# Optimization experiments

Hardware: AMD Instinct MI355X
Metric: run time of the kernel (lower is better)

The kernel has to match this reference:

```python
import jax, jax.numpy as jnp
import numpy as np

B, S, D, H = 4, 1024, 1024, 16
HD = D // H          # head space dim = 64
FF = 4 * D           # ffn hidden = 4096
EPS = 1e-6

# ---- Lorentz manifold helpers (curvature k=1: -t^2 + |s|^2 = -1) ----

def to_manifold(space):
    t = jnp.sqrt(jnp.sum(space * space, -1, keepdims=True) + 1.0)
    return jnp.concatenate([t, space], -1)

def l_inner(x, y):
    return -x[..., 0] * y[..., 0] + jnp.sum(x[..., 1:] * y[..., 1:], -1)

def project(z):
    # renormalize onto hyperboloid: z / sqrt(|<z,z>_L|)   (Lorentz midpoint / LResNet)
    d = jnp.sqrt(jnp.clip(-l_inner(z, z), EPS))
    return z / d[..., None]

def hyp_layernorm(x, g, b):
    s = x[..., 1:]
    mu = jnp.mean(s, -1, keepdims=True)
    var = jnp.var(s, -1, keepdims=True)
    s = (s - mu) * jax.lax.rsqrt(var + 1e-5) * g + b
    return to_manifold(s)

def apply_rope(xs, cos, sin):
    # xs [B,S,H,HD]; cos/sin [S,HD//2]; freqs broadcast as [1,S,1,HD//2]
    x2 = xs.reshape(*xs.shape[:-1], HD // 2, 2)
    c = cos[None, :, None, :]
    s = sin[None, :, None, :]
    xr = x2[..., 0] * c - x2[..., 1] * s
    xi = x2[..., 0] * s + x2[..., 1] * c
    return jnp.stack([xr, xi], -1).reshape(xs.shape)


def setup_inputs() -> dict:
    key = jax.random.key(0)
    ks = jax.random.split(key, 8)
    def w(k, shape, fan_in):
        return jax.random.normal(k, shape, jnp.float32) / np.sqrt(fan_in).astype(np.float32)
    x = to_manifold(0.5 * jax.random.normal(ks[0], (B, S, D), jnp.float32))
    pos = jnp.arange(S, dtype=jnp.float32)[:, None]
    inv = 1.0 / (10000.0 ** (jnp.arange(0, HD, 2, dtype=jnp.float32) / HD))
    ang = pos * inv[None, :]
    return {
        'x': x,
        'rope_cos': jnp.cos(ang), 'rope_sin': jnp.sin(ang),
        'norm1_g': jnp.ones((D,), jnp.float32), 'norm1_b': jnp.zeros((D,), jnp.float32),
        'Wq': w(ks[1], (H, D + 1, HD), D + 1), 'bq': jnp.zeros((H, HD), jnp.float32),
        'Wk': w(ks[2], (H, D + 1, HD), D + 1), 'bk': jnp.zeros((H, HD), jnp.float32),
        'Wv': w(ks[3], (H, D + 1, HD), D + 1), 'bv': jnp.zeros((H, HD), jnp.float32),
        'attn_scale': jnp.asarray(np.sqrt(HD), jnp.float32),
        'attn_bias': jnp.zeros((), jnp.float32),
        'Wo': w(ks[4], (H * (HD + 1), D), H * (HD + 1)), 'bo': jnp.zeros((D,), jnp.float32),
        'w_res1': jnp.asarray(1.0, jnp.float32),
        'norm2_g': jnp.ones((D,), jnp.float32), 'norm2_b': jnp.zeros((D,), jnp.float32),
        'W1': w(ks[5], (D + 1, FF), D + 1), 'b1': jnp.zeros((FF,), jnp.float32),
        'W2': w(ks[6], (FF + 1, D), FF + 1), 'b2': jnp.zeros((D,), jnp.float32),
        'w_res2': jnp.asarray(1.0, jnp.float32),
    }


def reference(x, rope_cos, rope_sin, norm1_g, norm1_b, Wq, bq, Wk, bk, Wv, bv,
              attn_scale, attn_bias, Wo, bo, w_res1, norm2_g, norm2_b,
              W1, b1, W2, b2, w_res2):
    # ---- pre-norm ----
    xn = hyp_layernorm(x, norm1_g, norm1_b)
    # ---- per-head Lorentz linear (space part), inline RoPE on q/k ----
    qs = jnp.einsum('bsd,hde->bshe', xn, Wq) + bq          # [B,S,H,HD]
    ksp = jnp.einsum('bsd,hde->bshe', xn, Wk) + bk
    vsp = jnp.einsum('bsd,hde->bshe', xn, Wv) + bv
    qs = apply_rope(qs, rope_cos, rope_sin)
    ksp = apply_rope(ksp, rope_cos, rope_sin)
    # hyperbolic normalization of q/k: unit space norm, time recomputed
    qs = qs * jax.lax.rsqrt(jnp.sum(qs * qs, -1, keepdims=True) + EPS)
    ksp = ksp * jax.lax.rsqrt(jnp.sum(ksp * ksp, -1, keepdims=True) + EPS)
    q = to_manifold(qs)                                    # [B,S,H,HD+1]
    k = to_manifold(ksp)
    v = to_manifold(vsp)
    # ---- curvature-aware scores: 2 + 2 <q,k>_L (neg sq Lorentz distance) ----
    sgn = jnp.concatenate([-jnp.ones((1,), q.dtype), jnp.ones((HD,), q.dtype)])
    cin = jnp.einsum('bshe,bthe->bhst', q * sgn, k)        # Minkowski inner [B,H,S,S]
    att = (2.0 + 2.0 * cin) / attn_scale + attn_bias
    P = jax.nn.softmax(att, axis=-1)
    # ---- Lorentz midpoint aggregation of values ----
    m = jnp.einsum('bhst,bthe->bshe', P, v)
    m = project(m)                                         # back onto hyperboloid
    # ---- heads concat + output Lorentz linear ----
    cat = m.reshape(B, S, H * (HD + 1))
    attn_out = to_manifold(cat @ Wo + bo)
    # ---- LResNet residual 1 ----
    x = project(x + w_res1 * attn_out)
    # ---- Lorentz FFN ----
    h = hyp_layernorm(x, norm2_g, norm2_b)
    h = to_manifold(jax.nn.gelu(h @ W1 + b1))
    mlp = to_manifold(h @ W2 + b2)
    # ---- LResNet residual 2 ----
    x = project(x + w_res2 * mlp)
    return x
```

## Files before the change

kernel.cpp:

```cpp
#include <hip/hip_runtime.h>
#include <hip/hip_bf16.h>

typedef __hip_bfloat16 bf16;
typedef __attribute__((ext_vector_type(8))) short short8;
typedef __attribute__((ext_vector_type(4))) float f32x4;

#define B_  4
#define S_  1024
#define H_  16
#define R_  4096

#define MBL 1048576L
#define OFF_WQKVT (0L)
#define OFF_X2    (0L)
#define OFF_WOT   (6L*MBL + MBL/2)
#define OFF_W1T   (9L*MBL)
#define OFF_W2T   (17L*MBL + MBL/2)
#define OFF_BIAS  (26L*MBL)
#define OFF_XNB   (27L*MBL)
#define OFF_MCAT  (27L*MBL)
#define OFF_MLP   (27L*MBL)
#define OFF_QPS   (36L*MBL)
#define OFF_ARAW  (36L*MBL)
#define OFF_QT    (44L*MBL)
#define OFF_KPS   (45L*MBL)
#define OFF_HBUF  (45L*MBL)
#define OFF_KT    (53L*MBL)
#define OFF_VT    (54L*MBL)
#define OFF_HHC   (54L*MBL)
#define OFF_HHBIG (54L*MBL)
#define BQKV 0
#define BOF  16384
#define B1F  32768
#define B2F  65536
#define W2R0 81920
#define RCF  98304
#define RSNF 262144
#define SCLF 409600
#define TACC 425984
#define FLAG 458752

__device__ __forceinline__ bf16  f2bf(float v) { return __float2bfloat16(v); }
__device__ __forceinline__ float bf2f(bf16 v)  { return __bfloat162float(v); }
__device__ __forceinline__ unsigned short bf2s(float v) {
  return __builtin_bit_cast(unsigned short, __float2bfloat16(v));
}
__device__ __forceinline__ float ldu(const void* p, long i, int isbf) {
  return isbf ? bf2f(((const bf16*)p)[i]) : ((const float*)p)[i];
}
__device__ __forceinline__ void stu(void* p, long i, float v, int isbf) {
  if (isbf) ((bf16*)p)[i] = f2bf(v);
  else      ((float*)p)[i] = v;
}
__device__ __forceinline__ float gelu_f(float v) {
  const float u = 0.7978845608028654f * (v + 0.044715f * v * v * v);
  const float e = __expf(fminf(2.f * u, 80.f));
  return 0.5f * v * (1.f + (e - 1.f) / (e + 1.f));
}
__device__ __forceinline__ float bfu_lo(unsigned u) {
  return __builtin_bit_cast(float, u << 16);
}
__device__ __forceinline__ float bfu_hi(unsigned u) {
  return __builtin_bit_cast(float, u & 0xFFFF0000u);
}

__device__ __forceinline__ void gload16(const bf16* g, short* l) {
  __builtin_amdgcn_global_load_lds(
      (const __attribute__((address_space(1))) unsigned int*)g,
      (__attribute__((address_space(3))) unsigned int*)l, 16, 0, 0);
}

__global__ void detect_kernel(const unsigned* __restrict__ g, int* __restrict__ flag) {
  if (threadIdx.x == 0) flag[0] = (g[0] == 0x3F803F80u) ? 1 : 0;
}

__global__ __launch_bounds__(256) void zero16_kernel(uint4* __restrict__ p, int n16) {
  int i = blockIdx.x * 256 + threadIdx.x;
  if (i < n16) p[i] = uint4{0, 0, 0, 0};
}

__global__ __launch_bounds__(256) void prep_misc(
    const void* bq, const void* bk, const void* bv, const void* bo, const void* b1,
    const void* b2, const void* W2, const void* rc, const void* rsn,
    const void* scl, const void* ab, const void* wr1, const void* wr2,
    char* bias_base, const int* __restrict__ flag) {
  const int isbf = flag[0];
  int i = blockIdx.x * 256 + threadIdx.x;
  float* bqkvf = (float*)(bias_base + BQKV);
  if (i < 1024)        { bqkvf[i] = ldu(bq, i, isbf); return; }
  if (i < 2048)        { bqkvf[i] = ldu(bk, i - 1024, isbf); return; }
  if (i < 3072)        { bqkvf[i] = ldu(bv, i - 2048, isbf); return; }
  if (i < 4096)        { ((float*)(bias_base + BOF))[i - 3072] = ldu(bo, i - 3072, isbf); return; }
  if (i < 8192)        { ((float*)(bias_base + B1F))[i - 4096] = ldu(b1, i - 4096, isbf); return; }
  if (i < 9216)        { ((float*)(bias_base + B2F))[i - 8192] = ldu(b2, i - 8192, isbf); return; }
  if (i < 10240)       { ((float*)(bias_base + W2R0))[i - 9216] = ldu(W2, i - 9216, isbf); return; }
  if (i < 10240+32768) { ((float*)(bias_base + RCF))[i - 10240] = ldu(rc, i - 10240, isbf); return; }
  if (i < 10240+65536) { ((float*)(bias_base + RSNF))[i - 43008] = ldu(rsn, i - 43008, isbf); return; }
  if (i == 75776)      { ((float*)(bias_base + SCLF))[0] = ldu(scl, 0, isbf); return; }
  if (i == 75777)      { ((float*)(bias_base + SCLF))[1] = ldu(ab, 0, isbf); return; }
  if (i == 75778)      { ((float*)(bias_base + SCLF))[2] = ldu(wr1, 0, isbf); return; }
  if (i == 75779)      { ((float*)(bias_base + SCLF))[3] = ldu(wr2, 0, isbf); return; }
}

__global__ __launch_bounds__(256) void transp_gen(const void* __restrict__ src, long src_off,
                                                  int src_rows, int src_ld,
                                                  bf16* __restrict__ dst, int dst_ld,
                                                  const int* __restrict__ flag) {
  const int isbf = flag[0];
  __shared__ float tl[64][65];
  int t = threadIdx.x, tx = t & 63, tg = t >> 6;
  int k0 = blockIdx.x * 64, n0 = blockIdx.y * 64;
  for (int i = tg; i < 64; i += 4) {
    int k = k0 + i;
    tl[i][tx] = (k < src_rows) ? ldu(src, src_off + (long)k * src_ld + n0 + tx, isbf) : 0.f;
  }
  __syncthreads();
  for (int i = tg; i < 64; i += 4) {
    int k = k0 + tx;
    if (k < dst_ld) dst[(long)(n0 + i) * dst_ld + k] = f2bf(tl[tx][i]);
  }
}

__global__ __launch_bounds__(256) void transp_qkv(const void* __restrict__ Wq,
                                                  const void* __restrict__ Wk,
                                                  const void* __restrict__ Wv,
                                                  bf16* __restrict__ dst,
                                                  const int* __restrict__ flag) {
  const int isbf = flag[0];
  __shared__ float tl[64][65];
  int t = threadIdx.x, tx = t & 63, tg = t >> 6;
  int k0 = blockIdx.x * 64;
  int z = blockIdx.y, mode = z >> 4, h = z & 15;
  const void* src = (mode == 0) ? Wq : (mode == 1) ? Wk : Wv;
  const long soff = (long)h * 1025 * 64;
  int base_n = mode * 1024 + h * 64;
  for (int i = tg; i < 64; i += 4) {
    int k = k0 + i;
    tl[i][tx] = (k < 1025) ? ldu(src, soff + (long)k * 64 + tx, isbf) : 0.f;
  }
  __syncthreads();
  for (int i = tg; i < 64; i += 4) {
    int k = k0 + tx;
    if (k < 1056) dst[(long)(base_n + i) * 1056 + k] = f2bf(tl[tx][i]);
  }
}

__global__ __launch_bounds__(256) void transp_wo(const void* __restrict__ src,
                                                 bf16* __restrict__ dst,
                                                 const int* __restrict__ flag) {
  const int isbf = flag[0];
  __shared__ float tl[64][65];
  int t = threadIdx.x, tx = t & 63, tg = t >> 6;
  int k0 = blockIdx.x * 64, n0 = blockIdx.y * 64;
  for (int i = tg; i < 64; i += 4) {
    int kp = k0 + i;
    int h = kp / 66, e = kp - h * 66;
    float v = 0.f;
    if (kp < 1056 && e < 65) v = ldu(src, (long)(h * 65 + e) * 1024 + n0 + tx, isbf);
    tl[i][tx] = v;
  }
  __syncthreads();
  for (int i = tg; i < 64; i += 4) {
    int kp = k0 + tx;
    if (kp < 1056) dst[(long)(n0 + i) * 1056 + kp] = f2bf(tl[tx][i]);
  }
}

__device__ __forceinline__ float bred_f(float v, float* sh) {
#pragma unroll
  for (int o = 32; o; o >>= 1) v += __shfl_xor(v, o);
  __syncthreads();
  if ((threadIdx.x & 63) == 0) sh[threadIdx.x >> 6] = v;
  __syncthreads();
  return sh[0] + sh[1] + sh[2] + sh[3];
}
__device__ __forceinline__ double bred_d(double v, double* sh) {
#pragma unroll
  for (int o = 32; o; o >>= 1) v += __shfl_xor(v, o);
  __syncthreads();
  if ((threadIdx.x & 63) == 0) sh[threadIdx.x >> 6] = v;
  __syncthreads();
  return sh[0] + sh[1] + sh[2] + sh[3];
}

__global__ __launch_bounds__(256) void ln_kernel(const void* __restrict__ x, int xtag,
                                                 const void* __restrict__ g,
                                                 const void* __restrict__ b,
                                                 bf16* __restrict__ out,
                                                 const int* __restrict__ flag) {
  const int isbf = flag[0];
  const int xb = (xtag == 2) ? isbf : xtag;
  __shared__ float red[4];
  const long base = (long)blockIdx.x * 1025;
  const long obase = (long)blockIdx.x * 1056;
  const int tid = threadIdx.x;
  float v[4];
#pragma unroll
  for (int i = 0; i < 4; i++) v[i] = ldu(x, base + 1 + tid * 4 + i, xb);
  float s = 0.f, s2 = 0.f;
#pragma unroll
  for (int i = 0; i < 4; i++) { s += v[i]; s2 += v[i] * v[i]; }
  s  = bred_f(s,  red);
  s2 = bred_f(s2, red);
  const float mu  = s * (1.f / 1024.f);
  const float var = s2 * (1.f / 1024.f) - mu * mu;
  const float rs  = rsqrtf(var + 1e-5f);
  float n[4], ns = 0.f;
#pragma unroll
  for (int i = 0; i < 4; i++) {
    const int e = tid * 4 + i;
    n[i] = (v[i] - mu) * rs * ldu(g, e, isbf) + ldu(b, e, isbf);
    ns += n[i] * n[i];
  }
  ns = bred_f(ns, red);
  if (tid == 0) out[obase] = f2bf(sqrtf(ns + 1.f));
#pragma unroll
  for (int i = 0; i < 4; i++) out[obase + 1 + tid * 4 + i] = f2bf(n[i]);
  if (tid < 31) out[obase + 1025 + tid] = f2bf(0.f);
}

template <int EPI, bool SS>
__global__ __launch_bounds__(256) void mfma_gemm(const bf16* __restrict__ A, int lda,
                                                 const bf16* __restrict__ Bw, int ldb, int K,
                                                 const float* __restrict__ bias,
                                                 void* __restrict__ Cv, int ldc, int accf,
                                                 float* __restrict__ tacc) {
  __shared__ __align__(16) short As[128 * 32];
  __shared__ __align__(16) short Bs[64 * 32];
  const int tid = threadIdx.x, lane = tid & 63, wv = tid >> 6;
  const int quad = lane >> 4, q15 = lane & 15;
  const int wave_m = wv & 1, wave_n = wv >> 1;
  const int n0 = blockIdx.x * 64, m0 = blockIdx.y * 128;
  const int sa0 = wv * 128 + lane, sa1 = sa0 + 64;
  const int ra0 = sa0 >> 2, ca0 = (sa0 & 3) ^ (ra0 & 3);
  const int ra1 = sa1 >> 2, ca1 = (sa1 & 3) ^ (ra1 & 3);
  const int rb = tid >> 2, cb = (tid & 3) ^ (rb & 3);
  const int kswz = (quad ^ (q15 & 3)) * 8;
  const bf16* pa0 = A + (long)(m0 + ra0) * lda + ca0 * 8;
  const bf16* pa1 = A + (long)(m0 + ra1) * lda + ca1 * 8;
  const bf16* pb  = Bw + (long)(n0 + rb) * ldb + cb * 8;
  f32x4 acc[4][2] = {};
  for (int k0 = 0; k0 < K; k0 += 32) {
    gload16(pa0, As + sa0 * 8);
    gload16(pa1, As + sa1 * 8);
    gload16(pb, Bs + tid * 8);
    pa0 += 32; pa1 += 32; pb += 32;
    __syncthreads();
    short8 af[4], bfr[2];
#pragma unroll
    for (int i = 0; i < 4; i++)
      af[i] = *(const short8*)(As + (wave_m * 64 + i * 16 + q15) * 32 + kswz);
#pragma unroll
    for (int i = 0; i < 2; i++)
      bfr[i] = *(const short8*)(Bs + (wave_n * 32 + i * 16 + q15) * 32 + kswz);
#pragma unroll
    for (int mi = 0; mi < 4; mi++)
#pragma unroll
      for (int ni = 0; ni < 2; ni++)
        acc[mi][ni] = __builtin_amdgcn_mfma_f32_16x16x32_bf16(af[mi], bfr[ni], acc[mi][ni], 0, 0, 0);
    __syncthreads();
  }
#pragma unroll
  for (int mi = 0; mi < 4; mi++) {
#pragma unroll
    for (int r = 0; r < 4; r++) {
      const int m = m0 + wave_m * 64 + mi * 16 + quad * 4 + r;
      float s2 = 0.f;
#pragma unroll
      for (int ni = 0; ni < 2; ni++) {
        const int n = n0 + wave_n * 32 + ni * 16 + q15;
        float v = acc[mi][ni][r] + (bias ? bias[n] : 0.f);
        const long idx = (long)m * ldc + n;
        if (EPI == 0) {
          float* Cf = (float*)Cv;
          if (accf) v += Cf[idx];
          Cf[idx] = v;
        } else if (EPI == 1) {
          ((bf16*)Cv)[idx] = f2bf(v);
        } else {
          v = gelu_f(v);
          ((bf16*)Cv)[idx] = f2bf(v);
        }
        if (SS) s2 += v * v;
      }
      if (SS) {
        s2 += __shfl_xor(s2, 1);
        s2 += __shfl_xor(s2, 2);
        s2 += __shfl_xor(s2, 4);
        s2 += __shfl_xor(s2, 8);
        if (q15 == 0) atomicAdd(tacc + m, s2);
      }
    }
  }
}

template <int EPI>
__global__ __launch_bounds__(256) void mfma_gemm128(const bf16* __restrict__ A, int lda,
                                                    const bf16* __restrict__ Bw, int ldb, int K,
                                                    const float* __restrict__ bias,
                                                    void* __restrict__ Cv, int ldc, int accf) {
  __shared__ __align__(16) short As[128 * 32];
  __shared__ __align__(16) short Bs[128 * 32];
  const int tid = threadIdx.x, lane = tid & 63, wv = tid >> 6;
  const int quad = lane >> 4, q15 = lane & 15;
  const int wave_m = wv & 1, wave_n = wv >> 1;
  const int n0 = blockIdx.x * 128, m0 = blockIdx.y * 128;
  const int s0 = wv * 128 + lane, s1 = s0 + 64;
  const int r0 = s0 >> 2, c0 = (s0 & 3) ^ (r0 & 3);
  const int r1 = s1 >> 2, c1 = (s1 & 3) ^ (r1 & 3);
  const int kswz = (quad ^ (q15 & 3)) * 8;
  const bf16* pa0 = A + (long)(m0 + r0) * lda + c0 * 8;
  const bf16* pa1 = A + (long)(m0 + r1) * lda + c1 * 8;
  const bf16* pb0 = Bw + (long)(n0 + r0) * ldb + c0 * 8;
  const bf16* pb1 = Bw + (long)(n0 + r1) * ldb + c1 * 8;
  f32x4 acc[4][4] = {};
  for (int k0 = 0; k0 < K; k0 += 32) {
    gload16(pa0, As + s0 * 8);
    gload16(pa1, As + s1 * 8);
    gload16(pb0, Bs + s0 * 8);
    gload16(pb1, Bs + s1 * 8);
    pa0 += 32; pa1 += 32; pb0 += 32; pb1 += 32;
    __syncthreads();
    short8 af[4], bfr[4];
#pragma unroll
    for (int i = 0; i < 4; i++) {
      af[i]  = *(const short8*)(As + (wave_m * 64 + i * 16 + q15) * 32 + kswz);
      bfr[i] = *(const short8*)(Bs + (wave_n * 64 + i * 16 + q15) * 32 + kswz);
    }
#pragma unroll
    for (int mi = 0; mi < 4; mi++)
#pragma unroll
      for (int ni = 0; ni < 4; ni++)
        acc[mi][ni] = __builtin_amdgcn_mfma_f32_16x16x32_bf16(af[mi], bfr[ni], acc[mi][ni], 0, 0, 0);
    __syncthreads();
  }
#pragma unroll
  for (int mi = 0; mi < 4; mi++) {
#pragma unroll
    for (int r = 0; r < 4; r++) {
      const int m = m0 + wave_m * 64 + mi * 16 + quad * 4 + r;
#pragma unroll
      for (int ni = 0; ni < 4; ni++) {
        const int n = n0 + wave_n * 64 + ni * 16 + q15;
        float v = acc[mi][ni][r] + (bias ? bias[n] : 0.f);
        const long idx = (long)m * ldc + n;
        if (EPI == 0) {
          float* Cf = (float*)Cv;
          if (accf) v += Cf[idx];
          Cf[idx] = v;
        } else if (EPI == 1) {
          ((bf16*)Cv)[idx] = f2bf(v);
        } else {
          ((bf16*)Cv)[idx] = f2bf(gelu_f(v));
        }
      }
    }
  }
}

__global__ __launch_bounds__(256) void gemm_qkv(const bf16* __restrict__ A,
                                                const bf16* __restrict__ Wt,
                                                const char* __restrict__ bias_base,
                                                bf16* __restrict__ qPs, float* __restrict__ qtc,
                                                bf16* __restrict__ kPs, float* __restrict__ ktc,
                                                bf16* __restrict__ vT) {
  __shared__ __align__(16) short As[128 * 32];
  __shared__ __align__(16) short Bs[128 * 32];
  const int tid = threadIdx.x, lane = tid & 63, wv = tid >> 6;
  const int quad = lane >> 4, q15 = lane & 15;
  const int wave_m = wv & 1, wave_n = wv >> 1;
  const int n0 = blockIdx.x * 128, m0 = blockIdx.y * 128;
  const int s0 = wv * 128 + lane, s1 = s0 + 64;
  const int r0 = s0 >> 2, c0 = (s0 & 3) ^ (r0 & 3);
  const int r1 = s1 >> 2, c1 = (s1 & 3) ^ (r1 & 3);
  const int kswz = (quad ^ (q15 & 3)) * 8;
  const float* bqkvf = (const float*)(bias_base + BQKV);
  const float* rcf   = (const float*)(bias_base + RCF);
  const float* rsnf  = (const float*)(bias_base + RSNF);
  const bf16* pa0 = A + (long)(m0 + r0) * 1056 + c0 * 8;
  const bf16* pa1 = A + (long)(m0 + r1) * 1056 + c1 * 8;
  const bf16* pb0 = Wt + (long)(n0 + r0) * 1056 + c0 * 8;
  const bf16* pb1 = Wt + (long)(n0 + r1) * 1056 + c1 * 8;
  f32x4 acc[4][4] = {};
  for (int k0 = 0; k0 < 1056; k0 += 32) {
    gload16(pa0, As + s0 * 8);
    gload16(pa1, As + s1 * 8);
    gload16(pb0, Bs + s0 * 8);
    gload16(pb1, Bs + s1 * 8);
    pa0 += 32; pa1 += 32; pb0 += 32; pb1 += 32;
    __syncthreads();
    short8 af[4], bfr[4];
#pragma unroll
    for (int i = 0; i < 4; i++) {
      af[i]  = *(const short8*)(As + (wave_m * 64 + i * 16 + q15) * 32 + kswz);
      bfr[i] = *(const short8*)(Bs + (wave_n * 64 + i * 16 + q15) * 32 + kswz);
    }
#pragma unroll
    for (int mi = 0; mi < 4; mi++)
#pragma unroll
      for (int ni = 0; ni < 4; ni++)
        acc[mi][ni] = __builtin_amdgcn_mfma_f32_16x16x32_bf16(af[mi], bfr[ni], acc[mi][ni], 0, 0, 0);
    __syncthreads();
  }
  const int hg = (n0 >> 6) + wave_n;
  const int mode = hg >> 4, h = hg & 15;
  const int nb = hg * 64;
#pragma unroll
  for (int mi = 0; mi < 4; mi++) {
#pragma unroll
    for (int r = 0; r < 4; r++) {
      const int m = m0 + wave_m * 64 + mi * 16 + quad * 4 + r;
      const int bb = m >> 10, s = m & 1023;
      const int bh = bb * H_ + h;
      float v[4];
#pragma unroll
      for (int ns = 0; ns < 4; ns++) v[ns] = acc[mi][ns][r] + bqkvf[nb + ns * 16 + q15];
      if (mode < 2) {
#pragma unroll
        for (int ns = 0; ns < 4; ns++) {
          const int eg = ns * 16 + q15;
          const int j = eg >> 1;
          const float c = rcf[s * 32 + j], sn = rsnf[s * 32 + j];
          const float p = __shfl_xor(v[ns], 1);
          v[ns] = ((eg & 1) == 0) ? (v[ns] * c - p * sn) : (p * sn + v[ns] * c);
        }
      }
      float ss = v[0] * v[0] + v[1] * v[1] + v[2] * v[2] + v[3] * v[3];
#pragma unroll
      for (int o = 8; o; o >>= 1) ss += __shfl_xor(ss, o);
      if (mode == 0) {
        const float sc = rsqrtf(ss + 1e-6f);
        const long rb = (long)(bh * 1024 + s) * 64;
#pragma unroll
        for (int ns = 0; ns < 4; ns++) qPs[rb + ns * 16 + q15] = f2bf(v[ns] * sc);
        if (q15 == 0) qtc[bh * 1024 + s] = sqrtf(ss / (ss + 1e-6f) + 1.f);
      } else if (mode == 1) {
        const float sc = rsqrtf(ss + 1e-6f);
        const long rb = (long)(bh * 1024 + s) * 64;
#pragma unroll
        for (int ns = 0; ns < 4; ns++) kPs[rb + ns * 16 + q15] = f2bf(v[ns] * sc);
        if (q15 == 0) ktc[bh * 1024 + s] = sqrtf(ss / (ss + 1e-6f) + 1.f);
      } else {
        const long vb = (long)bh * 81920;
#pragma unroll
        for (int ns = 0; ns < 4; ns++) vT[vb + (long)(1 + ns * 16 + q15) * 1024 + s] = f2bf(v[ns]);
        if (q15 == 0) vT[vb + s] = f2bf(sqrtf(ss + 1.f));
      }
    }
  }
}

__global__ __launch_bounds__(256) void attn_kernel(const bf16* __restrict__ qPs,
                                                   const float* __restrict__ qtc,
                                                   const bf16* __restrict__ kPs,
                                                   const float* __restrict__ ktc,
                                                   const bf16* __restrict__ vT,
                                                   const float* __restrict__ scalf,
                                                   bf16* __restrict__ mcat) {
  __shared__ __align__(16) short kbuf[64 * 72];
  __shared__ __align__(16) short vbuf[80 * 72];
  __shared__ __align__(16) short pbuf[64 * 72];
  __shared__ float tkl[64];
  const int tid = threadIdx.x, lane = tid & 63, wv = tid >> 6;
  const int quad = lane >> 4, q15 = lane & 15;
  const int id = blockIdx.x;
  const int cxd = id & 7, jj_ = id >> 3;
  const int bh = cxd * 8 + (jj_ & 7), qt_ = jj_ >> 3;
  const float inv_scale = 1.f / scalf[0];
  const long qrow = (long)(bh * 1024 + qt_ * 64 + wv * 16 + q15) * 64;
  const short8 aq0 = *(const short8*)(qPs + qrow + quad * 8);
  const short8 aq1 = *(const short8*)(qPs + qrow + 32 + quad * 8);
  float tqr[4];
#pragma unroll
  for (int r = 0; r < 4; r++) tqr[r] = qtc[bh * 1024 + qt_ * 64 + wv * 16 + quad * 4 + r];
  f32x4 out[5];
#pragma unroll
  for (int mt = 0; mt < 5; mt++) out[mt] = f32x4{0, 0, 0, 0};
  float lip[4] = {0.f, 0.f, 0.f, 0.f};
  const int srcl = (q15 >> 2) << 4;
  for (int kt = 0; kt < 16; kt++) {
    __syncthreads();
#pragma unroll
    for (int c = 0; c < 2; c++) {
      const int id2 = c * 256 + tid, row = id2 >> 3, off = id2 & 7;
      *(uint4*)(kbuf + row * 72 + off * 8) =
          *(const uint4*)(kPs + (long)(bh * 1024 + kt * 64 + row) * 64 + off * 8);
    }
#pragma unroll
    for (int c = 0; c < 3; c++) {
      const int id2 = c * 256 + tid;
      if (id2 < 640) {
        const int row = id2 >> 3, off = id2 & 7;
        *(uint4*)(vbuf + row * 72 + off * 8) =
            *(const uint4*)(vT + (long)bh * 81920 + (long)row * 1024 + kt * 64 + off * 8);
      }
    }
    if (tid < 64) tkl[tid] = ktc[bh * 1024 + kt * 64 + tid];
    __syncthreads();
    f32x4 sacc[4] = {f32x4{0,0,0,0}, f32x4{0,0,0,0}, f32x4{0,0,0,0}, f32x4{0,0,0,0}};
#pragma unroll
    for (int ns = 0; ns < 4; ns++) {
      short8 b0 = *(const short8*)(kbuf + (ns * 16 + q15) * 72 + quad * 8);
      short8 b1 = *(const short8*)(kbuf + (ns * 16 + q15) * 72 + 32 + quad * 8);
      sacc[ns] = __builtin_amdgcn_mfma_f32_16x16x32_bf16(aq0, b0, sacc[ns], 0, 0, 0);
      sacc[ns] = __builtin_amdgcn_mfma_f32_16x16x32_bf16(aq1, b1, sacc[ns], 0, 0, 0);
    }
#pragma unroll
    for (int ns = 0; ns < 4; ns++) {
      const float tk = tkl[ns * 16 + q15];
#pragma unroll
      for (int r = 0; r < 4; r++) {
        const float pv = __expf((2.f + 2.f * (sacc[ns][r] - tqr[r] * tk)) * inv_scale);
        lip[r] += pv;
        pbuf[(wv * 16 + quad * 4 + r) * 72 + ns * 16 + q15] = (short)bf2s(pv);
      }
    }
#pragma unroll
    for (int mt = 0; mt < 5; mt++)
#pragma unroll
      for (int kc = 0; kc < 2; kc++) {
        short8 av = *(const short8*)(vbuf + (mt * 16 + q15) * 72 + kc * 32 + quad * 8);
        short8 bp = *(const short8*)(pbuf + (wv * 16 + q15) * 72 + kc * 32 + quad * 8);
        out[mt] = __builtin_amdgcn_mfma_f32_16x16x32_bf16(av, bp, out[mt], 0, 0, 0);
      }
  }
  {
#pragma unroll
    for (int o = 8; o; o >>= 1)
#pragma unroll
      for (int r = 0; r < 4; r++) lip[r] += __shfl_xor(lip[r], o);
    float linv[4];
#pragma unroll
    for (int r = 0; r < 4; r++) linv[r] = 1.f / lip[r];
    const float t0 = __shfl(linv[0], srcl), t1 = __shfl(linv[1], srcl);
    const float t2 = __shfl(linv[2], srcl), t3 = __shfl(linv[3], srcl);
    const int rr = q15 & 3;
    const float lv = (rr == 0) ? t0 : (rr == 1) ? t1 : (rr == 2) ? t2 : t3;
#pragma unroll
    for (int mt = 0; mt < 5; mt++)
#pragma unroll
      for (int j = 0; j < 4; j++) out[mt][j] *= lv;
  }
  float part = 0.f;
#pragma unroll
  for (int mt = 0; mt < 5; mt++)
#pragma unroll
    for (int j = 0; j < 4; j++) {
      const int e = mt * 16 + quad * 4 + j;
      const float vv = out[mt][j] * out[mt][j];
      part += (e == 0) ? vv : -vv;
    }
  part += __shfl_xor(part, 16);
  part += __shfl_xor(part, 32);
  const float dinv = rsqrtf(fmaxf(part, 1e-6f));
  __syncthreads();
  short* obuf = vbuf;
  const int qrow_l = wv * 16 + q15;
#pragma unroll
  for (int mt = 0; mt < 5; mt++)
#pragma unroll
    for (int j = 0; j < 4; j++) {
      const int e = mt * 16 + quad * 4 + j;
      if (e <= 64) obuf[qrow_l * 72 + e] = (short)bf2s(out[mt][j] * dinv);
    }
  if (quad == 1) obuf[qrow_l * 72 + 65] = 0;
  __syncthreads();
  const int b = bh >> 4, h = bh & 15;
  const long outbase = ((long)b * 1024 + qt_ * 64) * 1056 + h * 66;
  for (int i = tid; i < 64 * 33; i += 256) {
    const int row = i / 33, p = i - row * 33;
    *(unsigned*)(mcat + outbase + (long)row * 1056 + p * 2) =
        *(const unsigned*)(obuf + row * 72 + p * 2);
  }
}

__global__ __launch_bounds__(256) void final_fix_kernel(const float* __restrict__ t_acc,
                                                        const float* __restrict__ w2r0,
                                                        const float* __restrict__ b2f,
                                                        float* __restrict__ mlp) {
  const int m = blockIdx.x;
  const float t = sqrtf(1.f + t_acc[m]);
  float* row = mlp + (long)m * 1024;
  for (int n = threadIdx.x; n < 1024; n += 256) row[n] += t * w2r0[n] + b2f[n];
}

__global__ __launch_bounds__(256) void final_fix_big(const bf16* __restrict__ hh,
                                                     const float* __restrict__ w2r0,
                                                     const float* __restrict__ b2f,
                                                     float* __restrict__ mlp) {
  __shared__ float red[4];
  const int m = blockIdx.x;
  const uint4* r4 = (const uint4*)(hh + (long)m * 4096);
  float ss = 0.f;
  for (int i = threadIdx.x; i < 512; i += 256) {
    const uint4 u = r4[i];
    const unsigned a[4] = {u.x, u.y, u.z, u.w};
#pragma unroll
    for (int j = 0; j < 4; j++) {
      const float lo = bfu_lo(a[j]), hi = bfu_hi(a[j]);
      ss += lo * lo + hi * hi;
    }
  }
  ss = bred_f(ss, red);
  const float t = sqrtf(1.f + ss);
  float* row = mlp + (long)m * 1024;
  for (int n = threadIdx.x; n < 1024; n += 256) row[n] += t * w2r0[n] + b2f[n];
}

__global__ __launch_bounds__(256) void res_project_kernel(
    const void* __restrict__ x, int xtag, const void* __restrict__ c, int ctag,
    const float* __restrict__ scalf, int widx, void* __restrict__ out, int otag,
    const int* __restrict__ flag) {
  const int isbf = flag[0];
  const int xb = (xtag == 2) ? isbf : xtag;
  const int cb2 = (ctag == 2) ? isbf : ctag;
  const int ob = (otag == 2) ? isbf : otag;
  __shared__ double red[4];
  const long bx = (long)blockIdx.x * 1025;
  const long bc = (long)blockIdx.x * 1024;
  const int tid = threadIdx.x;
  const double w = (double)scalf[widx];
  const float x0 = ldu(x, bx, xb);
  float xs[4], cv[4];
#pragma unroll
  for (int i = 0; i < 4; i++) {
    xs[i] = ldu(x, bx + 1 + tid * 4 + i, xb);
    cv[i] = ldu(c, bc + tid * 4 + i, cb2);
  }
  double cc = 0.0, xx = 0.0, xc = 0.0;
#pragma unroll
  for (int i = 0; i < 4; i++) {
    cc += (double)cv[i] * cv[i];
    xx += (double)xs[i] * xs[i];
    xc += (double)xs[i] * cv[i];
  }
  cc = bred_d(cc, red);
  xx = bred_d(xx, red);
  xc = bred_d(xc, red);
  const double t   = sqrt(1.0 + cc);
  const double lxx = (double)x0 * x0 - xx;
  const double xm  = -(double)x0 * t + xc;
  double d2 = lxx + w * w - 2.0 * w * xm;
  if (d2 < 1e-6) d2 = 1e-6;
  const double dinv = 1.0 / sqrt(d2);
  if (tid == 0) stu(out, bx, (float)(((double)x0 + w * t) * dinv), ob);
#pragma unroll
  for (int i = 0; i < 4; i++)
    stu(out, bx + 1 + tid * 4 + i, (float)(((double)xs[i] + w * cv[i]) * dinv), ob);
}

extern "C" void kernel_launch(void* const* d_in, const int* in_sizes, int n_in,
                              void* d_out, int out_size, void* d_ws, size_t ws_size,
                              hipStream_t stream) {
  char* w = (char*)d_ws;
  char* bias_base = w + OFF_BIAS;
  int* flag = (int*)(bias_base + FLAG);
  float* tacc = (float*)(bias_base + TACC);
  const float* scalf = (const float*)(bias_base + SCLF);
  const bool big = ws_size >= (size_t)92 * MBL;

  detect_kernel<<<1, 64, 0, stream>>>((const unsigned*)d_in[3], flag);
  zero16_kernel<<<4, 256, 0, stream>>>((uint4*)tacc, 1024);

  prep_misc<<<297, 256, 0, stream>>>(
      d_in[6], d_in[8], d_in[10], d_in[14], d_in[19], d_in[21], d_in[20], d_in[1],
      d_in[2], d_in[11], d_in[12], d_in[15], d_in[22], bias_base, flag);
  transp_qkv<<<dim3(17, 48), 256, 0, stream>>>(d_in[5], d_in[7], d_in[9],
                                               (bf16*)(w + OFF_WQKVT), flag);
  transp_wo<<<dim3(17, 16), 256, 0, stream>>>(d_in[13], (bf16*)(w + OFF_WOT), flag);
  transp_gen<<<dim3(17, 64), 256, 0, stream>>>(d_in[18], 0, 1025, 4096,
                                               (bf16*)(w + OFF_W1T), 1056, flag);
  transp_gen<<<dim3(64, 16), 256, 0, stream>>>(d_in[20], 1024, 4096, 1024,
                                               (bf16*)(w + OFF_W2T), 4096, flag);
  ln_kernel<<<R_, 256, 0, stream>>>(d_in[0], 2, d_in[3], d_in[4], (bf16*)(w + OFF_XNB), flag);

  gemm_qkv<<<dim3(24, 32), 256, 0, stream>>>(
      (const bf16*)(w + OFF_XNB), (const bf16*)(w + OFF_WQKVT), bias_base,
      (bf16*)(w + OFF_QPS), (float*)(w + OFF_QT), (bf16*)(w + OFF_KPS),
      (float*)(w + OFF_KT), (bf16*)(w + OFF_VT));
  attn_kernel<<<1024, 256, 0, stream>>>(
      (const bf16*)(w + OFF_QPS), (const float*)(w + OFF_QT), (const bf16*)(w + OFF_KPS),
      (const float*)(w + OFF_KT), (const bf16*)(w + OFF_VT), scalf, (bf16*)(w + OFF_MCAT));
  mfma_gemm<1, false><<<dim3(16, 32), 256, 0, stream>>>(
      (const bf16*)(w + OFF_MCAT), 1056, (const bf16*)(w + OFF_WOT), 1056, 1056,
      (const float*)(bias_base + BOF), w + OFF_ARAW, 1024, 0, nullptr);
  res_project_kernel<<<R_, 256, 0, stream>>>(d_in[0], 2, w + OFF_ARAW, 1, scalf, 2,
                                             w + OFF_X2, 1, flag);
  ln_kernel<<<R_, 256, 0, stream>>>(w + OFF_X2, 1, d_in[16], d_in[17],
                                    (bf16*)(w + OFF_HBUF), flag);
  if (big) {
    mfma_gemm128<2><<<dim3(32, 32), 256, 0, stream>>>(
        (const bf16*)(w + OFF_HBUF), 1056, (const bf16*)(w + OFF_W1T), 1056, 1056,
        (const float*)(bias_base + B1F), w + OFF_HHBIG, 4096, 0);
    mfma_gemm<0, false><<<dim3(16, 32), 256, 0, stream>>>(
        (const bf16*)(w + OFF_HHBIG), 4096, (const bf16*)(w + OFF_W2T), 4096, 4096,
        nullptr, w + OFF_MLP, 1024, 0, nullptr);
    final_fix_big<<<R_, 256, 0, stream>>>((const bf16*)(w + OFF_HHBIG),
                                          (const float*)(bias_base + W2R0),
                                          (const float*)(bias_base + B2F),
                                          (float*)(w + OFF_MLP));
  } else {
    for (int c = 0; c < 4; c++) {
      mfma_gemm<2, true><<<dim3(16, 32), 256, 0, stream>>>(
          (const bf16*)(w + OFF_HBUF), 1056, (const bf16*)(w + OFF_W1T) + (long)c * 1024 * 1056,
          1056, 1056, (const float*)(bias_base + B1F) + c * 1024, w + OFF_HHC, 1024, 0, tacc);
      mfma_gemm<0, false><<<dim3(16, 32), 256, 0, stream>>>(
          (const bf16*)(w + OFF_HHC), 1024, (const bf16*)(w + OFF_W2T) + c * 1024, 4096, 1024,
          nullptr, w + OFF_MLP, 1024, c > 0 ? 1 : 0, nullptr);
    }
    final_fix_kernel<<<R_, 256, 0, stream>>>(tacc, (const float*)(bias_base + W2R0),
                                             (const float*)(bias_base + B2F),
                                             (float*)(w + OFF_MLP));
  }
  res_project_kernel<<<R_, 256, 0, stream>>>(w + OFF_X2, 1, w + OFF_MLP, 0, scalf, 3,
                                             d_out, 2, flag);
}
```

Measured before the change: 531.4 us.

## Process two K-slices per barrier in MFMA GEMMs and pad K to 1088

The GEMM main loops now load two 32-wide K slices into separate shared buffers per iteration. This halves the number of __syncthreads pairs and lets more MFMAs issue between barriers. To keep K a multiple of 64, the padded inner dimension grows from 1056 to 1088, so the weight transposes, layernorm padding and attention output write extra zero columns. This adds roughly 3% redundant MACs on those GEMMs, and the workspace offsets are rearranged to fit the larger buffers.

```diff
diff --git a/kernel.cpp b/kernel.cpp
--- a/kernel.cpp
+++ b/kernel.cpp
@@ -9,26 +9,28 @@
 #define S_  1024
 #define H_  16
 #define R_  4096
+#define LD_ 1088
 
 #define MBL 1048576L
 #define OFF_WQKVT (0L)
+#define OFF_WOT   (6684672L)
 #define OFF_X2    (0L)
-#define OFF_WOT   (6L*MBL + MBL/2)
 #define OFF_W1T   (9L*MBL)
-#define OFF_W2T   (17L*MBL + MBL/2)
+#define OFF_W2T   (18L*MBL)
 #define OFF_BIAS  (26L*MBL)
-#define OFF_XNB   (27L*MBL)
-#define OFF_MCAT  (27L*MBL)
-#define OFF_MLP   (27L*MBL)
+#define OFF_XNB   (27L*MBL + MBL/2)
+#define OFF_MCAT  OFF_XNB
+#define OFF_HBUF  OFF_XNB
 #define OFF_QPS   (36L*MBL)
-#define OFF_ARAW  (36L*MBL)
-#define OFF_QT    (44L*MBL)
-#define OFF_KPS   (45L*MBL)
-#define OFF_HBUF  (45L*MBL)
-#define OFF_KT    (53L*MBL)
-#define OFF_VT    (54L*MBL)
-#define OFF_HHC   (54L*MBL)
-#define OFF_HHBIG (54L*MBL)
+#define OFF_ARAW  OFF_QPS
+#define OFF_KPS   (44L*MBL)
+#define OFF_VT    (52L*MBL)
+#define OFF_QT    (62L*MBL)
+#define OFF_KT    (62L*MBL + 262144L)
+#define OFF_HHBIG (44L*MBL)
+#define OFF_MLPB  (76L*MBL)
+#define OFF_HHC   (36L*MBL)
+#define OFF_MLPF  (44L*MBL)
 #define BQKV 0
 #define BOF  16384
 #define B1F  32768
@@ -141,7 +143,7 @@
   __syncthreads();
   for (int i = tg; i < 64; i += 4) {
     int k = k0 + tx;
-    if (k < 1056) dst[(long)(base_n + i) * 1056 + k] = f2bf(tl[tx][i]);
+    if (k < LD_) dst[(long)(base_n + i) * LD_ + k] = f2bf(tl[tx][i]);
   }
 }
 
@@ -154,15 +156,17 @@
   int k0 = blockIdx.x * 64, n0 = blockIdx.y * 64;
   for (int i = tg; i < 64; i += 4) {
     int kp = k0 + i;
-    int h = kp / 66, e = kp - h * 66;
     float v = 0.f;
-    if (kp < 1056 && e < 65) v = ldu(src, (long)(h * 65 + e) * 1024 + n0 + tx, isbf);
+    if (kp < 1056) {
+      int h = kp / 66, e = kp - h * 66;
+      if (e < 65) v = ldu(src, (long)(h * 65 + e) * 1024 + n0 + tx, isbf);
+    }
     tl[i][tx] = v;
   }
   __syncthreads();
   for (int i = tg; i < 64; i += 4) {
     int kp = k0 + tx;
-    if (kp < 1056) dst[(long)(n0 + i) * 1056 + kp] = f2bf(tl[tx][i]);
+    if (kp < LD_) dst[(long)(n0 + i) * LD_ + kp] = f2bf(tl[tx][i]);
   }
 }
 
@@ -192,7 +196,7 @@
   const int xb = (xtag == 2) ? isbf : xtag;
   __shared__ float red[4];
   const long base = (long)blockIdx.x * 1025;
-  const long obase = (long)blockIdx.x * 1056;
+  const long obase = (long)blockIdx.x * LD_;
   const int tid = threadIdx.x;
   float v[4];
 #pragma unroll
@@ -216,7 +220,7 @@
   if (tid == 0) out[obase] = f2bf(sqrtf(ns + 1.f));
 #pragma unroll
   for (int i = 0; i < 4; i++) out[obase + 1 + tid * 4 + i] = f2bf(n[i]);
-  if (tid < 31) out[obase + 1025 + tid] = f2bf(0.f);
+  if (tid < 63) out[obase + 1025 + tid] = f2bf(0.f);
 }
 
 template <int EPI, bool SS>
@@ -225,8 +229,8 @@
                                                  const float* __restrict__ bias,
                                                  void* __restrict__ Cv, int ldc, int accf,
                                                  float* __restrict__ tacc) {
-  __shared__ __align__(16) short As[128 * 32];
-  __shared__ __align__(16) short Bs[64 * 32];
+  __shared__ __align__(16) short As[2][128 * 32];
+  __shared__ __align__(16) short Bs[2][64 * 32];
   const int tid = threadIdx.x, lane = tid & 63, wv = tid >> 6;
   const int quad = lane >> 4, q15 = lane & 15;
   const int wave_m = wv & 1, wave_n = wv >> 1;
@@ -240,24 +244,30 @@
   const bf16* pa1 = A + (long)(m0 + ra1) * lda + ca1 * 8;
   const bf16* pb  = Bw + (long)(n0 + rb) * ldb + cb * 8;
   f32x4 acc[4][2] = {};
-  for (int k0 = 0; k0 < K; k0 += 32) {
-    gload16(pa0, As + sa0 * 8);
-    gload16(pa1, As + sa1 * 8);
-    gload16(pb, Bs + tid * 8);
-    pa0 += 32; pa1 += 32; pb += 32;
+  for (int k0 = 0; k0 < K; k0 += 64) {
+#pragma unroll
+    for (int p = 0; p < 2; p++) {
+      gload16(pa0 + p * 32, As[p] + sa0 * 8);
+      gload16(pa1 + p * 32, As[p] + sa1 * 8);
+      gload16(pb + p * 32, Bs[p] + tid * 8);
+    }
+    pa0 += 64; pa1 += 64; pb += 64;
     __syncthreads();
-    short8 af[4], bfr[2];
-#pragma unroll
-    for (int i = 0; i < 4; i++)
-      af[i] = *(const short8*)(As + (wave_m * 64 + i * 16 + q15) * 32 + kswz);
-#pragma unroll
-    for (int i = 0; i < 2; i++)
-      bfr[i] = *(const short8*)(Bs + (wave_n * 32 + i * 16 + q15) * 32 + kswz);
-#pragma unroll
-    for (int mi = 0; mi < 4; mi++)
-#pragma unroll
-      for (int ni = 0; ni < 2; ni++)
-        acc[mi][ni] = __builtin_amdgcn_mfma_f32_16x16x32_bf16(af[mi], bfr[ni], acc[mi][ni], 0, 0, 0);
+#pragma unroll
+    for (int p = 0; p < 2; p++) {
+      short8 af[4], bfr[2];
+#pragma unroll
+      for (int i = 0; i < 4; i++)
+        af[i] = *(const short8*)(As[p] + (wave_m * 64 + i * 16 + q15) * 32 + kswz);
+#pragma unroll
+      for (int i = 0; i < 2; i++)
+        bfr[i] = *(const short8*)(Bs[p] + (wave_n * 32 + i * 16 + q15) * 32 + kswz);
+#pragma unroll
+      for (int mi = 0; mi < 4; mi++)
+#pragma unroll
+        for (int ni = 0; ni < 2; ni++)
+          acc[mi][ni] = __builtin_amdgcn_mfma_f32_16x16x32_bf16(af[mi], bfr[ni], acc[mi][ni], 0, 0, 0);
+    }
     __syncthreads();
   }
 #pragma unroll
@@ -299,8 +309,8 @@
                                                     const bf16* __restrict__ Bw, int ldb, int K,
                                                     const float* __restrict__ bias,
                                                     void* __restrict__ Cv, int ldc, int accf) {
-  __shared__ __align__(16) short As[128 * 32];
-  __shared__ __align__(16) short Bs[128 * 32];
+  __shared__ __align__(16) short As[2][128 * 32];
+  __shared__ __align__(16) short Bs[2][128 * 32];
   const int tid = threadIdx.x, lane = tid & 63, wv = tid >> 6;
   const int quad = lane >> 4, q15 = lane & 15;
   const int wave_m = wv & 1, wave_n = wv >> 1;
@@ -314,24 +324,30 @@
   const bf16* pb0 = Bw + (long)(n0 + r0) * ldb + c0 * 8;
   const bf16* pb1 = Bw + (long)(n0 + r1) * ldb + c1 * 8;
   f32x4 acc[4][4] = {};
-  for (int k0 = 0; k0 < K; k0 += 32) {
-    gload16(pa0, As + s0 * 8);
-    gload16(pa1, As + s1 * 8);
-    gload16(pb0, Bs + s0 * 8);
-    gload16(pb1, Bs + s1 * 8);
-    pa0 += 32; pa1 += 32; pb0 += 32; pb1 += 32;
+  for (int k0 = 0; k0 < K; k0 += 64) {
+#pragma unroll
+    for (int p = 0; p < 2; p++) {
+      gload16(pa0 + p * 32, As[p] + s0 * 8);
+      gload16(pa1 + p * 32, As[p] + s1 * 8);
+      gload16(pb0 + p * 32, Bs[p] + s0 * 8);
+      gload16(pb1 + p * 32, Bs[p] + s1 * 8);
+    }
+    pa0 += 64; pa1 += 64; pb0 += 64; pb1 += 64;
     __syncthreads();
-    short8 af[4], bfr[4];
-#pragma unroll
-    for (int i = 0; i < 4; i++) {
-      af[i]  = *(const short8*)(As + (wave_m * 64 + i * 16 + q15) * 32 + kswz);
-      bfr[i] = *(const short8*)(Bs + (wave_n * 64 + i * 16 + q15) * 32 + kswz);
-    }
-#pragma unroll
-    for (int mi = 0; mi < 4; mi++)
-#pragma unroll
-      for (int ni = 0; ni < 4; ni++)
-        acc[mi][ni] = __builtin_amdgcn_mfma_f32_16x16x32_bf16(af[mi], bfr[ni], acc[mi][ni], 0, 0, 0);
+#pragma unroll
+    for (int p = 0; p < 2; p++) {
+      short8 af[4], bfr[4];
+#pragma unroll
+      for (int i = 0; i < 4; i++) {
+        af[i]  = *(const short8*)(As[p] + (wave_m * 64 + i * 16 + q15) * 32 + kswz);
+        bfr[i] = *(const short8*)(Bs[p] + (wave_n * 64 + i * 16 + q15) * 32 + kswz);
+      }
+#pragma unroll
+      for (int mi = 0; mi < 4; mi++)
+#pragma unroll
+        for (int ni = 0; ni < 4; ni++)
+          acc[mi][ni] = __builtin_amdgcn_mfma_f32_16x16x32_bf16(af[mi], bfr[ni], acc[mi][ni], 0, 0, 0);
+    }
     __syncthreads();
   }
 #pragma unroll
@@ -364,8 +380,8 @@
                                                 bf16* __restrict__ qPs, float* __restrict__ qtc,
                                                 bf16* __restrict__ kPs, float* __restrict__ ktc,
                                                 bf16* __restrict__ vT) {
-  __shared__ __align__(16) short As[128 * 32];
-  __shared__ __align__(16) short Bs[128 * 32];
+  __shared__ __align__(16) short As[2][128 * 32];
+  __shared__ __align__(16) short Bs[2][128 * 32];
   const int tid = threadIdx.x, lane = tid & 63, wv = tid >> 6;
   const int quad = lane >> 4, q15 = lane & 15;
   const int wave_m = wv & 1, wave_n = wv >> 1;
@@ -377,29 +393,35 @@
   const float* bqkvf = (const float*)(bias_base + BQKV);
   const float* rcf   = (const float*)(bias_base + RCF);
   const float* rsnf  = (const float*)(bias_base + RSNF);
-  const bf16* pa0 = A + (long)(m0 + r0) * 1056 + c0 * 8;
-  const bf16* pa1 = A + (long)(m0 + r1) * 1056 + c1 * 8;
-  const bf16* pb0 = Wt + (long)(n0 + r0) * 1056 + c0 * 8;
-  const bf16* pb1 = Wt + (long)(n0 + r1) * 1056 + c1 * 8;
+  const bf16* pa0 = A + (long)(m0 + r0) * LD_ + c0 * 8;
+  const bf16* pa1 = A + (long)(m0 + r1) * LD_ + c1 * 8;
+  const bf16* pb0 = Wt + (long)(n0 + r0) * LD_ + c0 * 8;
+  const bf16* pb1 = Wt + (long)(n0 + r1) * LD_ + c1 * 8;
   f32x4 acc[4][4] = {};
-  for (int k0 = 0; k0 < 1056; k0 += 32) {
-    gload16(pa0, As + s0 * 8);
-    gload16(pa1, As + s1 * 8);
-    gload16(pb0, Bs + s0 * 8);
-    gload16(pb1, Bs + s1 * 8);
-    pa0 += 32; pa1 += 32; pb0 += 32; pb1 += 32;
+  for (int k0 = 0; k0 < LD_; k0 += 64) {
+#pragma unroll
+    for (int p = 0; p < 2; p++) {
+      gload16(pa0 + p * 32, As[p] + s0 * 8);
+      gload16(pa1 + p * 32, As[p] + s1 * 8);
+      gload16(pb0 + p * 32, Bs[p] + s0 * 8);
+      gload16(pb1 + p * 32, Bs[p] + s1 * 8);
+    }
+    pa0 += 64; pa1 += 64; pb0 += 64; pb1 += 64;
     __syncthreads();
-    short8 af[4], bfr[4];
-#pragma unroll
-    for (int i = 0; i < 4; i++) {
-      af[i]  = *(const short8*)(As + (wave_m * 64 + i * 16 + q15) * 32 + kswz);
-      bfr[i] = *(const short8*)(Bs + (wave_n * 64 + i * 16 + q15) * 32 + kswz);
-    }
-#pragma unroll
-    for (int mi = 0; mi < 4; mi++)
-#pragma unroll
-      for (int ni = 0; ni < 4; ni++)
-        acc[mi][ni] = __builtin_amdgcn_mfma_f32_16x16x32_bf16(af[mi], bfr[ni], acc[mi][ni], 0, 0, 0);
+#pragma unroll
+    for (int p = 0; p < 2; p++) {
+      short8 af[4], bfr[4];
+#pragma unroll
+      for (int i = 0; i < 4; i++) {
+        af[i]  = *(const short8*)(As[p] + (wave_m * 64 + i * 16 + q15) * 32 + kswz);
+        bfr[i] = *(const short8*)(Bs[p] + (wave_n * 64 + i * 16 + q15) * 32 + kswz);
+      }
+#pragma unroll
+      for (int mi = 0; mi < 4; mi++)
+#pragma unroll
+        for (int ni = 0; ni < 4; ni++)
+          acc[mi][ni] = __builtin_amdgcn_mfma_f32_16x16x32_bf16(af[mi], bfr[ni], acc[mi][ni], 0, 0, 0);
+    }
     __syncthreads();
   }
   const int hg = (n0 >> 6) + wave_n;
@@ -430,15 +452,15 @@
       for (int o = 8; o; o >>= 1) ss += __shfl_xor(ss, o);
       if (mode == 0) {
         const float sc = rsqrtf(ss + 1e-6f);
-        const long rb = (long)(bh * 1024 + s) * 64;
-#pragma unroll
-        for (int ns = 0; ns < 4; ns++) qPs[rb + ns * 16 + q15] = f2bf(v[ns] * sc);
+        const long rb2 = (long)(bh * 1024 + s) * 64;
+#pragma unroll
+        for (int ns = 0; ns < 4; ns++) qPs[rb2 + ns * 16 + q15] = f2bf(v[ns] * sc);
         if (q15 == 0) qtc[bh * 1024 + s] = sqrtf(ss / (ss + 1e-6f) + 1.f);
       } else if (mode == 1) {
         const float sc = rsqrtf(ss + 1e-6f);
-        const long rb = (long)(bh * 1024 + s) * 64;
-#pragma unroll
-        for (int ns = 0; ns < 4; ns++) kPs[rb + ns * 16 + q15] = f2bf(v[ns] * sc);
+        const long rb2 = (long)(bh * 1024 + s) * 64;
+#pragma unroll
+        for (int ns = 0; ns < 4; ns++) kPs[rb2 + ns * 16 + q15] = f2bf(v[ns] * sc);
         if (q15 == 0) ktc[bh * 1024 + s] = sqrtf(ss / (ss + 1e-6f) + 1.f);
       } else {
         const long vb = (long)bh * 81920;
@@ -566,11 +588,18 @@
   if (quad == 1) obuf[qrow_l * 72 + 65] = 0;
   __syncthreads();
   const int b = bh >> 4, h = bh & 15;
-  const long outbase = ((long)b * 1024 + qt_ * 64) * 1056 + h * 66;
+  const long outbase = ((long)b * 1024 + qt_ * 64) * LD_ + h * 66;
   for (int i = tid; i < 64 * 33; i += 256) {
     const int row = i / 33, p = i - row * 33;
-    *(unsigned*)(mcat + outbase + (long)row * 1056 + p * 2) =
+    *(unsigned*)(mcat + outbase + (long)row * LD_ + p * 2) =
         *(const unsigned*)(obuf + row * 72 + p * 2);
+  }
+  if (h == 15) {
+    const long zb = ((long)b * 1024 + qt_ * 64) * LD_ + 1056;
+    for (int i = tid; i < 64 * 16; i += 256) {
+      const int row = i >> 4, p = i & 15;
+      *(unsigned*)(mcat + zb + (long)row * LD_ + p * 2) = 0u;
+    }
   }
 }
 
@@ -658,6 +687,7 @@
   float* tacc = (float*)(bias_base + TACC);
   const float* scalf = (const float*)(bias_base + SCLF);
   const bool big = ws_size >= (size_t)92 * MBL;
+  char* mlp_off = big ? (w + OFF_MLPB) : (w + OFF_MLPF);
 
   detect_kernel<<<1, 64, 0, stream>>>((const unsigned*)d_in[3], flag);
   zero16_kernel<<<4, 256, 0, stream>>>((uint4*)tacc, 1024);
@@ -669,7 +699,7 @@
                                                (bf16*)(w + OFF_WQKVT), flag);
   transp_wo<<<dim3(17, 16), 256, 0, stream>>>(d_in[13], (bf16*)(w + OFF_WOT), flag);
   transp_gen<<<dim3(17, 64), 256, 0, stream>>>(d_in[18], 0, 1025, 4096,
-                                               (bf16*)(w + OFF_W1T), 1056, flag);
+                                               (bf16*)(w + OFF_W1T), LD_, flag);
   transp_gen<<<dim3(64, 16), 256, 0, stream>>>(d_in[20], 1024, 4096, 1024,
                                                (bf16*)(w + OFF_W2T), 4096, flag);
   ln_kernel<<<R_, 256, 0, stream>>>(d_in[0], 2, d_in[3], d_in[4], (bf16*)(w + OFF_XNB), flag);
@@ -682,7 +712,7 @@
       (const bf16*)(w + OFF_QPS), (const float*)(w + OFF_QT), (const bf16*)(w + OFF_KPS),
       (const float*)(w + OFF_KT), (const bf16*)(w + OFF_VT), scalf, (bf16*)(w + OFF_MCAT));
   mfma_gemm<1, false><<<dim3(16, 32), 256, 0, stream>>>(
-      (const bf16*)(w + OFF_MCAT), 1056, (const bf16*)(w + OFF_WOT), 1056, 1056,
+      (const bf16*)(w + OFF_MCAT), LD_, (const bf16*)(w + OFF_WOT), LD_, LD_,
       (const float*)(bias_base + BOF), w + OFF_ARAW, 1024, 0, nullptr);
   res_project_kernel<<<R_, 256, 0, stream>>>(d_in[0], 2, w + OFF_ARAW, 1, scalf, 2,
                                              w + OFF_X2, 1, flag);
@@ -690,28 +720,28 @@
                                     (bf16*)(w + OFF_HBUF), flag);
   if (big) {
     mfma_gemm128<2><<<dim3(32, 32), 256, 0, stream>>>(
-        (const bf16*)(w + OFF_HBUF), 1056, (const bf16*)(w + OFF_W1T), 1056, 1056,
+        (const bf16*)(w + OFF_HBUF), LD_, (const bf16*)(w + OFF_W1T), LD_, LD_,
         (const float*)(bias_base + B1F), w + OFF_HHBIG, 4096, 0);
     mfma_gemm<0, false><<<dim3(16, 32), 256, 0, stream>>>(
         (const bf16*)(w + OFF_HHBIG), 4096, (const bf16*)(w + OFF_W2T), 4096, 4096,
-        nullptr, w + OFF_MLP, 1024, 0, nullptr);
+        nullptr, mlp_off, 1024, 0, nullptr);
     final_fix_big<<<R_, 256, 0, stream>>>((const bf16*)(w + OFF_HHBIG),
                                           (const float*)(bias_base + W2R0),
                                           (const float*)(bias_base + B2F),
-                                          (float*)(w + OFF_MLP));
+                                          (float*)mlp_off);
   } else {
     for (int c = 0; c < 4; c++) {
       mfma_gemm<2, true><<<dim3(16, 32), 256, 0, stream>>>(
-          (const bf16*)(w + OFF_HBUF), 1056, (const bf16*)(w + OFF_W1T) + (long)c * 1024 * 1056,
-          1056, 1056, (const float*)(bias_base + B1F) + c * 1024, w + OFF_HHC, 1024, 0, tacc);
+          (const bf16*)(w + OFF_HBUF), LD_, (const bf16*)(w + OFF_W1T) + (long)c * 1024 * LD_,
+          LD_, LD_, (const float*)(bias_base + B1F) + c * 1024, w + OFF_HHC, 1024, 0, tacc);
       mfma_gemm<0, false><<<dim3(16, 32), 256, 0, stream>>>(
           (const bf16*)(w + OFF_HHC), 1024, (const bf16*)(w + OFF_W2T) + c * 1024, 4096, 1024,
-          nullptr, w + OFF_MLP, 1024, c > 0 ? 1 : 0, nullptr);
+          nullptr, mlp_off, 1024, c > 0 ? 1 : 0, nullptr);
     }
     final_fix_kernel<<<R_, 256, 0, stream>>>(tacc, (const float*)(bias_base + W2R0),
                                              (const float*)(bias_base + B2F),
-                                             (float*)(w + OFF_MLP));
-  }
-  res_project_kernel<<<R_, 256, 0, stream>>>(w + OFF_X2, 1, w + OFF_MLP, 0, scalf, 3,
+                                             (float*)mlp_off);
+  }
+  res_project_kernel<<<R_, 256, 0, stream>>>(w + OFF_X2, 1, mlp_off, 0, scalf, 3,
                                              d_out, 2, flag);
 }
```

New measurement: 512.6 us. 3.5% less time.
